# Optimization experiments

Hardware: AMD Instinct MI355X
Metric: run time of the kernel (lower is better)

Reference implementation:

```python
import jax, jax.numpy as jnp
import numpy as np

NUM_STEPS = 8  # fixed-step RK4 stand-in for adaptive DormandPrince(atol=1e-5)
B, D, C, H = 8192, 508, 1, 256
DIN = D + C + 1  # state + conditional + time


def _mlp(h, w0, b0, w1, b1, w2, b2):
    h = jnp.tanh(h @ w0 + b0)
    h = jnp.tanh(h @ w1 + b1)
    return h @ w2 + b2


def setup_inputs() -> dict:
    key = jax.random.key(0)
    ks = jax.random.split(key, 6)
    sc = lambda k, shape, fan: jax.random.normal(k, shape, jnp.float32) / np.sqrt(fan)
    return {
        "x": jax.random.normal(ks[0], (B, D), jnp.float32),
        "cond": jax.random.uniform(ks[1], (B, C), jnp.float32),
        "eps": jax.random.normal(ks[2], (B, D), jnp.float32),  # Hutchinson probe
        "w0": sc(ks[3], (DIN, H), DIN),
        "b0": jnp.zeros((H,), jnp.float32),
        "w1": sc(ks[4], (H, H), H),
        "b1": jnp.zeros((H,), jnp.float32),
        "w2": sc(ks[5], (H, D), H),
        "b2": jnp.zeros((D,), jnp.float32),
    }


def reference(x, cond, eps, w0, b0, w1, b1, w2, b2):
    """FFJORD bijector forward: integrate dx/dt = f(t, x, cond) from t=0 to 1
    with augmented Hutchinson trace estimate d(logdet)/dt = eps^T (df/dx) eps.
    Returns (y, log_det_jacobian_estimate)."""
    dt = jnp.float32(1.0 / NUM_STEPS)

    def dyn(t, y):
        def f(y_):
            tcol = jnp.full((y_.shape[0], 1), t, y_.dtype)
            return _mlp(jnp.concatenate([y_, cond, tcol], axis=-1),
                        w0, b0, w1, b1, w2, b2)
        fy, vjp_fn = jax.vjp(f, y)
        (etJ,) = vjp_fn(eps)           # eps^T J
        tr = jnp.sum(etJ * eps, -1)    # eps^T J eps  -> [B]
        return fy, tr

    def step(carry, i):
        y, ld = carry
        t = i * dt
        k1, l1 = dyn(t, y)
        k2, l2 = dyn(t + 0.5 * dt, y + 0.5 * dt * k1)
        k3, l3 = dyn(t + 0.5 * dt, y + 0.5 * dt * k2)
        k4, l4 = dyn(t + dt, y + dt * k3)
        y = y + (dt / 6.0) * (k1 + 2.0 * k2 + 2.0 * k3 + k4)
        ld = ld + (dt / 6.0) * (l1 + 2.0 * l2 + 2.0 * l3 + l4)
        return (y, ld), None

    init = (x, jnp.zeros((x.shape[0],), x.dtype))
    (y, ld), _ = jax.lax.scan(step, init, jnp.arange(NUM_STEPS, dtype=x.dtype))
    return y, ld
```

## Files before the change

### kernel.cpp

```cpp
#include <hip/hip_runtime.h>
#include <math.h>

namespace {

constexpr int Bn = 8192;
constexpr int Dn = 508;
constexpr int Hn = 256;
constexpr int NSTEPS = 8;
constexpr int Kp = 512;
constexpr float DT = 1.f / NSTEPS;
constexpr float DT6 = DT / 6.f;

typedef __attribute__((ext_vector_type(8))) short short8v;
typedef __attribute__((ext_vector_type(4))) float f32x4;

__device__ __forceinline__ short f2b(float f) {
  union { float f; unsigned u; } v; v.f = f;
  unsigned r = v.u + 0x7fffu + ((v.u >> 16) & 1u);
  return (short)(r >> 16);
}
__device__ __forceinline__ float b2f(short s) {
  union { unsigned u; float f; } v;
  v.u = ((unsigned)(unsigned short)s) << 16;
  return v.f;
}
__device__ __forceinline__ unsigned pk2(short lo, short hi) {
  return ((unsigned)(unsigned short)lo) | (((unsigned)(unsigned short)hi) << 16);
}
__device__ __forceinline__ float upk_lo(unsigned p) {
  union { unsigned u; float f; } v; v.u = p << 16; return v.f;
}
__device__ __forceinline__ float upk_hi(unsigned p) {
  union { unsigned u; float f; } v; v.u = p & 0xffff0000u; return v.f;
}
__device__ __forceinline__ float ftanh(float x) {
  x = fminf(fmaxf(x, -12.f), 12.f);
  const float e = __expf(2.f * x);
  return __fdividef(e - 1.f, e + 1.f);
}

template <int KT>
__device__ __forceinline__ void gemm_bb(const short* __restrict__ A, int lda,
                                        const short* __restrict__ Bt, int ldb,
                                        int row0, int col0, int lane,
                                        f32x4 acc[2][2]) {
  const int r = lane & 15, g = lane >> 4;
  const short* a0p = A + (size_t)(row0 + r) * lda + g * 8;
  const short* a1p = A + (size_t)(row0 + 16 + r) * lda + g * 8;
  const short* b0p = Bt + (size_t)(col0 + r) * ldb + g * 8;
  const short* b1p = Bt + (size_t)(col0 + 16 + r) * ldb + g * 8;
#pragma unroll
  for (int kt = 0; kt < KT; ++kt) {
    const short8v a0 = *(const short8v*)(a0p + kt * 32);
    const short8v a1 = *(const short8v*)(a1p + kt * 32);
    const short8v b0 = *(const short8v*)(b0p + kt * 32);
    const short8v b1 = *(const short8v*)(b1p + kt * 32);
    acc[0][0] = __builtin_amdgcn_mfma_f32_16x16x32_bf16(a0, b0, acc[0][0], 0, 0, 0);
    acc[0][1] = __builtin_amdgcn_mfma_f32_16x16x32_bf16(a0, b1, acc[0][1], 0, 0, 0);
    acc[1][0] = __builtin_amdgcn_mfma_f32_16x16x32_bf16(a1, b0, acc[1][0], 0, 0, 0);
    acc[1][1] = __builtin_amdgcn_mfma_f32_16x16x32_bf16(a1, b1, acc[1][1], 0, 0, 0);
  }
}

#define GEMM_PROLOGUE()                                     \
  const int tid = threadIdx.x, wid = tid >> 6, lane = tid & 63; \
  const int row0 = blockIdx.y * 64 + (wid >> 1) * 32;       \
  const int col0 = blockIdx.x * 64 + (wid & 1) * 32;        \
  const int rq = (lane >> 4) * 4, cc = lane & 15;           \
  const f32x4 z4 = {0.f, 0.f, 0.f, 0.f};                    \
  f32x4 acc[2][2] = {{z4, z4}, {z4, z4}};


__global__ __launch_bounds__(256) void k_cast_bf(const float* __restrict__ src, int R,
                                                 int C, short* __restrict__ dst, int ldd) {
  const int total = R * ldd;
  for (int idx = blockIdx.x * 256 + threadIdx.x; idx < total; idx += gridDim.x * 256) {
    const int r = idx / ldd, c = idx - r * ldd;
    dst[idx] = (c < C) ? f2b(src[(size_t)r * C + c]) : (short)0;
  }
}

__global__ __launch_bounds__(256) void k_transpose_bf(const float* __restrict__ src, int K,
                                                      int N, short* __restrict__ dst,
                                                      int Nd, int ldd) {
  const int total = Nd * ldd;
  for (int idx = blockIdx.x * 256 + threadIdx.x; idx < total; idx += gridDim.x * 256) {
    const int n = idx / ldd, k = idx - n * ldd;
    dst[idx] = (k < K && n < N) ? f2b(src[(size_t)k * N + n]) : (short)0;
  }
}

__global__ __launch_bounds__(256) void k_c0(const float* __restrict__ w0,
                                            const float* __restrict__ b2,
                                            float* __restrict__ c0) {
  const int n = threadIdx.x;
  float s = 0.f;
#pragma unroll 8
  for (int d = 0; d < Dn; ++d) s += b2[d] * w0[(size_t)d * Hn + n];
  c0[n] = s;
}

__global__ __launch_bounds__(256) void k_w20t(const short* __restrict__ w0T,
                                              const short* __restrict__ w2b,
                                              short* __restrict__ w20T) {
  GEMM_PROLOGUE();
  gemm_bb<16>(w0T, Kp, w2b, Kp, row0, col0, lane, acc);
#pragma unroll
  for (int i = 0; i < 2; ++i)
#pragma unroll
    for (int j = 0; j < 2; ++j)
#pragma unroll
      for (int q = 0; q < 4; ++q)
        w20T[(size_t)(row0 + i * 16 + rq + q) * Hn + col0 + j * 16 + cc] =
            f2b(acc[i][j][q]);
}

__global__ __launch_bounds__(256) void k_ginitx(const float* __restrict__ Af,
                                                const short* __restrict__ Bt,
                                                const float* __restrict__ cond,
                                                const float* __restrict__ w0c,
                                                float* __restrict__ zout) {
  GEMM_PROLOGUE();
  const int g = lane >> 4;
  const float* a0r = Af + (size_t)(row0 + cc) * Dn;
  const float* a1r = Af + (size_t)(row0 + 16 + cc) * Dn;
  const short* b0p = Bt + (size_t)(col0 + cc) * Kp + g * 8;
  const short* b1p = Bt + (size_t)(col0 + 16 + cc) * Kp + g * 8;
#pragma unroll
  for (int kt = 0; kt < 16; ++kt) {
    const int k = kt * 32 + g * 8;
    short8v a0v, a1v;
#pragma unroll
    for (int h = 0; h < 2; ++h) {
      const int k4 = k + h * 4;
      float4 fa = make_float4(0.f, 0.f, 0.f, 0.f);
      float4 fb = make_float4(0.f, 0.f, 0.f, 0.f);
      if (k4 < Dn) {
        fa = *(const float4*)(a0r + k4);
        fb = *(const float4*)(a1r + k4);
      }
      a0v[h * 4 + 0] = f2b(fa.x); a0v[h * 4 + 1] = f2b(fa.y);
      a0v[h * 4 + 2] = f2b(fa.z); a0v[h * 4 + 3] = f2b(fa.w);
      a1v[h * 4 + 0] = f2b(fb.x); a1v[h * 4 + 1] = f2b(fb.y);
      a1v[h * 4 + 2] = f2b(fb.z); a1v[h * 4 + 3] = f2b(fb.w);
    }
    const short8v b0v = *(const short8v*)(b0p + kt * 32);
    const short8v b1v = *(const short8v*)(b1p + kt * 32);
    acc[0][0] = __builtin_amdgcn_mfma_f32_16x16x32_bf16(a0v, b0v, acc[0][0], 0, 0, 0);
    acc[0][1] = __builtin_amdgcn_mfma_f32_16x16x32_bf16(a0v, b1v, acc[0][1], 0, 0, 0);
    acc[1][0] = __builtin_amdgcn_mfma_f32_16x16x32_bf16(a1v, b0v, acc[1][0], 0, 0, 0);
    acc[1][1] = __builtin_amdgcn_mfma_f32_16x16x32_bf16(a1v, b1v, acc[1][1], 0, 0, 0);
  }
#pragma unroll
  for (int i = 0; i < 2; ++i)
#pragma unroll
    for (int j = 0; j < 2; ++j)
#pragma unroll
      for (int q = 0; q < 4; ++q) {
        const int row = row0 + i * 16 + rq + q;
        const int col = col0 + j * 16 + cc;
        zout[(size_t)row * Hn + col] = acc[i][j][q] + cond[row] * w0c[col];
      }
}

__global__ __launch_bounds__(256) void k_giniteps(const float* __restrict__ Af,
                                                  const short* __restrict__ BtU,
                                                  const short* __restrict__ BtG,
                                                  short* __restrict__ uout,
                                                  short* __restrict__ gout) {
  GEMM_PROLOGUE();
  f32x4 acc2[2][2] = {{z4, z4}, {z4, z4}};
  const int g = lane >> 4;
  const float* a0r = Af + (size_t)(row0 + cc) * Dn;
  const float* a1r = Af + (size_t)(row0 + 16 + cc) * Dn;
  const short* u0p = BtU + (size_t)(col0 + cc) * Kp + g * 8;
  const short* u1p = BtU + (size_t)(col0 + 16 + cc) * Kp + g * 8;
  const short* g0p = BtG + (size_t)(col0 + cc) * Kp + g * 8;
  const short* g1p = BtG + (size_t)(col0 + 16 + cc) * Kp + g * 8;
#pragma unroll
  for (int kt = 0; kt < 16; ++kt) {
    const int k = kt * 32 + g * 8;
    short8v a0v, a1v;
#pragma unroll
    for (int h = 0; h < 2; ++h) {
      const int k4 = k + h * 4;
      float4 fa = make_float4(0.f, 0.f, 0.f, 0.f);
      float4 fb = make_float4(0.f, 0.f, 0.f, 0.f);
      if (k4 < Dn) {
        fa = *(const float4*)(a0r + k4);
        fb = *(const float4*)(a1r + k4);
      }
      a0v[h * 4 + 0] = f2b(fa.x); a0v[h * 4 + 1] = f2b(fa.y);
      a0v[h * 4 + 2] = f2b(fa.z); a0v[h * 4 + 3] = f2b(fa.w);
      a1v[h * 4 + 0] = f2b(fb.x); a1v[h * 4 + 1] = f2b(fb.y);
      a1v[h * 4 + 2] = f2b(fb.z); a1v[h * 4 + 3] = f2b(fb.w);
    }
    const short8v bu0 = *(const short8v*)(u0p + kt * 32);
    const short8v bu1 = *(const short8v*)(u1p + kt * 32);
    const short8v bg0 = *(const short8v*)(g0p + kt * 32);
    const short8v bg1 = *(const short8v*)(g1p + kt * 32);
    acc[0][0] = __builtin_amdgcn_mfma_f32_16x16x32_bf16(a0v, bu0, acc[0][0], 0, 0, 0);
    acc[0][1] = __builtin_amdgcn_mfma_f32_16x16x32_bf16(a0v, bu1, acc[0][1], 0, 0, 0);
    acc[1][0] = __builtin_amdgcn_mfma_f32_16x16x32_bf16(a1v, bu0, acc[1][0], 0, 0, 0);
    acc[1][1] = __builtin_amdgcn_mfma_f32_16x16x32_bf16(a1v, bu1, acc[1][1], 0, 0, 0);
    acc2[0][0] = __builtin_amdgcn_mfma_f32_16x16x32_bf16(a0v, bg0, acc2[0][0], 0, 0, 0);
    acc2[0][1] = __builtin_amdgcn_mfma_f32_16x16x32_bf16(a0v, bg1, acc2[0][1], 0, 0, 0);
    acc2[1][0] = __builtin_amdgcn_mfma_f32_16x16x32_bf16(a1v, bg0, acc2[1][0], 0, 0, 0);
    acc2[1][1] = __builtin_amdgcn_mfma_f32_16x16x32_bf16(a1v, bg1, acc2[1][1], 0, 0, 0);
  }
#pragma unroll
  for (int i = 0; i < 2; ++i)
#pragma unroll
    for (int j = 0; j < 2; ++j)
#pragma unroll
      for (int q = 0; q < 4; ++q) {
        const int row = row0 + i * 16 + rq + q;
        const int col = col0 + j * 16 + cc;
        uout[(size_t)row * Hn + col] = f2b(acc[i][j][q]);
        gout[(size_t)row * Hn + col] = f2b(acc2[i][j][q]);
      }
}

__global__ __launch_bounds__(256) void k_fragpack(const short* __restrict__ src,
                                                  short* __restrict__ dst, int total) {
  for (int idx = blockIdx.x * 256 + threadIdx.x; idx < total; idx += gridDim.x * 256) {
    const int j = idx & 7;
    const int l = (idx >> 3) & 63;
    const int ks = (idx >> 9) & 7;
    const int c16 = idx >> 12;
    dst[idx] = src[(size_t)(c16 * 16 + (l & 15)) * 256 + ks * 32 + (l >> 4) * 8 + j];
  }
}


__device__ __forceinline__ int swz(int row, int col) {
  return (row * 256 + col) ^ ((row & 7) << 3);
}

__global__ __launch_bounds__(512) void k_mega(
    const float* __restrict__ zg, const short* __restrict__ u_g,
    const short* __restrict__ g2_g, const short* __restrict__ w1P,
    const short* __restrict__ w20P, const short* __restrict__ w2P,
    const float* __restrict__ b0, const float* __restrict__ w0t,
    const float* __restrict__ b1, const float* __restrict__ c0,
    const float* __restrict__ b2, const float* __restrict__ x,
    float* __restrict__ yout, float* __restrict__ ldout) {
  __shared__ short As[32 * 256];
  __shared__ short h1s[16 * 256];
  __shared__ float red[16][8];

  const int tid = threadIdx.x;
  const int w = tid >> 6, lane = tid & 63;
  const int cc = lane & 15, g = lane >> 4, rq = g * 4;
  const int r0 = blockIdx.x * 16;
  const int cb = w * 32;

  float b0c[2], w0tc[2], b1c[2], c0c[2];
#pragma unroll
  for (int nt = 0; nt < 2; ++nt) {
    const int col = cb + nt * 16 + cc;
    b0c[nt] = b0[col];
    w0tc[nt] = w0t[col];
    b1c[nt] = b1[col];
    c0c[nt] = c0[col];
  }

  const short* w1base = w1P + (size_t)(2 * w) * 4096 + lane * 8;
  const short* w20base = w20P + (size_t)(2 * w) * 4096 + lane * 8;

  const size_t gbase = (size_t)(r0 + rq) * Hn + cb + cc;

  float z_[2][4], kzp[2][4], kza[2][4], hs[2][4], tr_[4];
  unsigned u_pk[2][2], g2_pk[2][2];
#pragma unroll
  for (int nt = 0; nt < 2; ++nt) {
    const size_t i0 = gbase + nt * 16;
#pragma unroll
    for (int q = 0; q < 4; ++q) {
      z_[nt][q] = zg[i0 + (size_t)q * Hn];
      kzp[nt][q] = 0.f;
      hs[nt][q] = 0.f;
    }
    u_pk[nt][0] = pk2(u_g[i0], u_g[i0 + Hn]);
    u_pk[nt][1] = pk2(u_g[i0 + 2 * Hn], u_g[i0 + 3 * Hn]);
    g2_pk[nt][0] = pk2(g2_g[i0], g2_g[i0 + Hn]);
    g2_pk[nt][1] = pk2(g2_g[i0 + 2 * Hn], g2_g[i0 + 3 * Hn]);
  }
#pragma unroll
  for (int q = 0; q < 4; ++q) tr_[q] = 0.f;

  const f32x4 zero4 = {0.f, 0.f, 0.f, 0.f};

#pragma unroll 1
  for (int e = 0; e < 4 * NSTEPS; ++e) {
    const int j = e & 3, s = e >> 2;
    const float oj = (j == 0) ? 0.f : ((j == 3) ? 1.f : 0.5f);
    const float aj = (j == 0) ? 0.f : ((j == 3) ? DT : 0.5f * DT);
    const float mj = (j == 1 || j == 2) ? 2.f : 1.f;
    const float tval = ((float)s + oj) * DT;

#pragma unroll
    for (int nt = 0; nt < 2; ++nt)
#pragma unroll
      for (int q = 0; q < 4; ++q) {
        const int row = rq + q;
        const int colh = cb + nt * 16 + cc;
        const float pre = z_[nt][q] + aj * kzp[nt][q] + b0c[nt] + tval * w0tc[nt];
        const float h = ftanh(pre);
        const float uq = (q & 1) ? upk_hi(u_pk[nt][q >> 1]) : upk_lo(u_pk[nt][q >> 1]);
        As[swz(row, colh)] = f2b(h);
        As[swz(16 + row, colh)] = f2b((1.f - h * h) * uq);
      }
    __syncthreads();

    {
      f32x4 acc[2][2] = {{zero4, zero4}, {zero4, zero4}};
#pragma unroll
      for (int ks = 0; ks < 8; ++ks) {
        const short8v b0v = *(const short8v*)(w1base + ks * 512);
        const short8v b1v = *(const short8v*)(w1base + 4096 + ks * 512);
        const short8v a0 = *(const short8v*)(As + swz(cc, g * 8 + ks * 32));
        const short8v a1 = *(const short8v*)(As + swz(16 + cc, g * 8 + ks * 32));
        acc[0][0] = __builtin_amdgcn_mfma_f32_16x16x32_bf16(a0, b0v, acc[0][0], 0, 0, 0);
        acc[0][1] = __builtin_amdgcn_mfma_f32_16x16x32_bf16(a0, b1v, acc[0][1], 0, 0, 0);
        acc[1][0] = __builtin_amdgcn_mfma_f32_16x16x32_bf16(a1, b0v, acc[1][0], 0, 0, 0);
        acc[1][1] = __builtin_amdgcn_mfma_f32_16x16x32_bf16(a1, b1v, acc[1][1], 0, 0, 0);
      }
#pragma unroll
      for (int nt = 0; nt < 2; ++nt)
#pragma unroll
        for (int q = 0; q < 4; ++q) {
          const float v = ftanh(acc[0][nt][q] + b1c[nt]);
          const float g2q =
              (q & 1) ? upk_hi(g2_pk[nt][q >> 1]) : upk_lo(g2_pk[nt][q >> 1]);
          tr_[q] += (DT6 * mj) * g2q * (1.f - v * v) * acc[1][nt][q];
          h1s[swz(rq + q, cb + nt * 16 + cc)] = f2b(v);
          hs[nt][q] += mj * v;
        }
    }
    __syncthreads();

    {
      f32x4 acc2[2] = {zero4, zero4};
#pragma unroll
      for (int ks = 0; ks < 8; ++ks) {
        const short8v b0v = *(const short8v*)(w20base + ks * 512);
        const short8v b1v = *(const short8v*)(w20base + 4096 + ks * 512);
        const short8v a = *(const short8v*)(h1s + swz(cc, g * 8 + ks * 32));
        acc2[0] = __builtin_amdgcn_mfma_f32_16x16x32_bf16(a, b0v, acc2[0], 0, 0, 0);
        acc2[1] = __builtin_amdgcn_mfma_f32_16x16x32_bf16(a, b1v, acc2[1], 0, 0, 0);
      }
#pragma unroll
      for (int nt = 0; nt < 2; ++nt)
#pragma unroll
        for (int q = 0; q < 4; ++q) {
          const float kzv = acc2[nt][q] + c0c[nt];
          if (j == 0) {
            kza[nt][q] = kzv;
            kzp[nt][q] = kzv;
          } else if (j < 3) {
            kza[nt][q] += mj * kzv;
            kzp[nt][q] = kzv;
          } else {
            z_[nt][q] += DT6 * (kza[nt][q] + kzv);
          }
        }
    }
  }

#pragma unroll
  for (int nt = 0; nt < 2; ++nt)
#pragma unroll
    for (int q = 0; q < 4; ++q)
      As[swz(rq + q, cb + nt * 16 + cc)] = f2b(hs[nt][q]);
  __syncthreads();
  {
    const short* w2base = w2P + (size_t)(4 * w) * 4096 + lane * 8;
    f32x4 facc[4] = {zero4, zero4, zero4, zero4};
#pragma unroll
    for (int ks = 0; ks < 8; ++ks) {
      const short8v a = *(const short8v*)(As + swz(cc, g * 8 + ks * 32));
#pragma unroll
      for (int nt = 0; nt < 4; ++nt) {
        const short8v bv = *(const short8v*)(w2base + nt * 4096 + ks * 512);
        facc[nt] = __builtin_amdgcn_mfma_f32_16x16x32_bf16(a, bv, facc[nt], 0, 0, 0);
      }
    }
#pragma unroll
    for (int nt = 0; nt < 4; ++nt) {
      const int colo = w * 64 + nt * 16 + cc;
      if (colo < Dn) {
        const float b2c = b2[colo];
#pragma unroll
        for (int q = 0; q < 4; ++q) {
          const size_t ix = (size_t)(r0 + rq + q) * Dn + colo;
          yout[ix] = x[ix] + DT6 * facc[nt][q] + b2c;
        }
      }
    }
  }

#pragma unroll
  for (int q = 0; q < 4; ++q) {
    float v = tr_[q];
    v += __shfl_xor(v, 1);
    v += __shfl_xor(v, 2);
    v += __shfl_xor(v, 4);
    v += __shfl_xor(v, 8);
    if (cc == 0) red[rq + q][w] = v;
  }
  __syncthreads();
  if (tid < 16) {
    float t = 0.f;
#pragma unroll
    for (int ww = 0; ww < 8; ++ww) t += red[tid][ww];
    ldout[r0 + tid] = t;
  }
}

}

extern "C" void kernel_launch(void* const* d_in, const int* in_sizes, int n_in,
                              void* d_out, int out_size, void* d_ws, size_t ws_size,
                              hipStream_t stream) {
  const float* x = (const float*)d_in[0];
  const float* cond = (const float*)d_in[1];
  const float* eps = (const float*)d_in[2];
  const float* w0 = (const float*)d_in[3];
  const float* b0 = (const float*)d_in[4];
  const float* w1 = (const float*)d_in[5];
  const float* b1 = (const float*)d_in[6];
  const float* w2 = (const float*)d_in[7];
  const float* b2 = (const float*)d_in[8];
  const float* w0c = w0 + (size_t)508 * Hn;
  const float* w0t = w0 + (size_t)509 * Hn;

  const size_t BD = (size_t)Bn * Dn, BH = (size_t)Bn * Hn;
  char* p = (char*)d_ws;
  auto alloc_f = [&](size_t n) { float* r = (float*)p; p += n * 4; return r; };
  auto alloc_s = [&](size_t n) { short* r = (short*)p; p += ((n * 2 + 15) & ~15ull); return r; };

  float* zg = alloc_f(BH);
  float* c0 = alloc_f(256);
  short* u_g = alloc_s(BH);
  short* g2_g = alloc_s(BH);
  short* w0T = alloc_s(256 * 512);
  short* w1T = alloc_s(256 * 256);
  short* w2b = alloc_s(256 * 512);
  short* w2T = alloc_s(512 * 256);
  short* w20T = alloc_s(256 * 256);
  short* w1P = alloc_s(256 * 256);
  short* w20P = alloc_s(256 * 256);
  short* w2P = alloc_s(512 * 256);

  float* yout = (float*)d_out;
  float* ldout = (float*)d_out + BD;

  const dim3 blk(256);
  const dim3 gH(Hn / 64, Bn / 64);
  const dim3 gW(4, 4);

  k_cast_bf<<<512, blk, 0, stream>>>(w2, Hn, Dn, w2b, Kp);
  k_transpose_bf<<<256, blk, 0, stream>>>(w1, Hn, Hn, w1T, Hn, Hn);
  k_transpose_bf<<<512, blk, 0, stream>>>(w0, Dn, Hn, w0T, Hn, Kp);
  k_transpose_bf<<<512, blk, 0, stream>>>(w2, Hn, Dn, w2T, Kp, Hn);
  k_c0<<<1, blk, 0, stream>>>(w0, b2, c0);
  k_w20t<<<gW, blk, 0, stream>>>(w0T, w2b, w20T);
  k_ginitx<<<gH, blk, 0, stream>>>(x, w0T, cond, w0c, zg);
  k_giniteps<<<gH, blk, 0, stream>>>(eps, w0T, w2b, u_g, g2_g);
  k_fragpack<<<256, blk, 0, stream>>>(w1T, w1P, 256 * 256);
  k_fragpack<<<256, blk, 0, stream>>>(w20T, w20P, 256 * 256);
  k_fragpack<<<512, blk, 0, stream>>>(w2T, w2P, 512 * 256);

  k_mega<<<dim3(Bn / 16), dim3(512), 0, stream>>>(zg, u_g, g2_g, w1P, w20P,
                                                  w2P, b0, w0t, b1, c0, b2, x,
                                                  yout, ldout);
}
```

Measured before the change: 306.5 us.

## Process 32 rows per block to reuse weight fragments across two row tiles

Each block of the fused ODE kernel now handles 32 batch rows instead of 16, so every weight fragment loaded from global memory for the W1 and W20 MFMAs serves two row tiles. The running hidden-state sum moves from registers into a padded shared-memory array to hold down register pressure from the doubled per-thread state. The grid halves to 256 blocks, which may leave some compute units idle or lower occupancy, and the larger LDS footprint (about 33KB for hsum alone) limits how many blocks fit per CU.

```diff
diff --git a/kernel.cpp b/kernel.cpp
--- a/kernel.cpp
+++ b/kernel.cpp
@@ -237,6 +237,8 @@
   return (row * 256 + col) ^ ((row & 7) << 3);
 }
 
+constexpr int HP = 258;
+
 __global__ __launch_bounds__(512) void k_mega(
     const float* __restrict__ zg, const short* __restrict__ u_g,
     const short* __restrict__ g2_g, const short* __restrict__ w1P,
@@ -245,14 +247,15 @@
     const float* __restrict__ b1, const float* __restrict__ c0,
     const float* __restrict__ b2, const float* __restrict__ x,
     float* __restrict__ yout, float* __restrict__ ldout) {
-  __shared__ short As[32 * 256];
-  __shared__ short h1s[16 * 256];
-  __shared__ float red[16][8];
+  __shared__ short As[64 * 256];
+  __shared__ short h1s[32 * 256];
+  __shared__ float hsum[32 * HP];
+  __shared__ float red[32][8];
 
   const int tid = threadIdx.x;
   const int w = tid >> 6, lane = tid & 63;
   const int cc = lane & 15, g = lane >> 4, rq = g * 4;
-  const int r0 = blockIdx.x * 16;
+  const int r0 = blockIdx.x * 32;
   const int cb = w * 32;
 
   float b0c[2], w0tc[2], b1c[2], c0c[2];
@@ -270,24 +273,29 @@
 
   const size_t gbase = (size_t)(r0 + rq) * Hn + cb + cc;
 
-  float z_[2][4], kzp[2][4], kza[2][4], hs[2][4], tr_[4];
-  unsigned u_pk[2][2], g2_pk[2][2];
-#pragma unroll
-  for (int nt = 0; nt < 2; ++nt) {
-    const size_t i0 = gbase + nt * 16;
-#pragma unroll
-    for (int q = 0; q < 4; ++q) {
-      z_[nt][q] = zg[i0 + (size_t)q * Hn];
-      kzp[nt][q] = 0.f;
-      hs[nt][q] = 0.f;
-    }
-    u_pk[nt][0] = pk2(u_g[i0], u_g[i0 + Hn]);
-    u_pk[nt][1] = pk2(u_g[i0 + 2 * Hn], u_g[i0 + 3 * Hn]);
-    g2_pk[nt][0] = pk2(g2_g[i0], g2_g[i0 + Hn]);
-    g2_pk[nt][1] = pk2(g2_g[i0 + 2 * Hn], g2_g[i0 + 3 * Hn]);
-  }
-#pragma unroll
-  for (int q = 0; q < 4; ++q) tr_[q] = 0.f;
+  float z_[2][2][4], kzp[2][2][4], kza[2][2][4], tr_[2][4];
+  unsigned u_pk[2][2][2], g2_pk[2][2][2];
+#pragma unroll
+  for (int rb = 0; rb < 2; ++rb)
+#pragma unroll
+    for (int nt = 0; nt < 2; ++nt) {
+      const size_t i0 = gbase + (size_t)(rb * 16) * Hn + nt * 16;
+#pragma unroll
+      for (int q = 0; q < 4; ++q) {
+        z_[rb][nt][q] = zg[i0 + (size_t)q * Hn];
+        kzp[rb][nt][q] = 0.f;
+      }
+      u_pk[rb][nt][0] = pk2(u_g[i0], u_g[i0 + Hn]);
+      u_pk[rb][nt][1] = pk2(u_g[i0 + 2 * Hn], u_g[i0 + 3 * Hn]);
+      g2_pk[rb][nt][0] = pk2(g2_g[i0], g2_g[i0 + Hn]);
+      g2_pk[rb][nt][1] = pk2(g2_g[i0 + 2 * Hn], g2_g[i0 + 3 * Hn]);
+    }
+#pragma unroll
+  for (int rb = 0; rb < 2; ++rb)
+#pragma unroll
+    for (int q = 0; q < 4; ++q) tr_[rb][q] = 0.f;
+
+  for (int i = tid; i < 32 * HP; i += 512) hsum[i] = 0.f;
 
   const f32x4 zero4 = {0.f, 0.f, 0.f, 0.f};
 
@@ -300,27 +308,33 @@
     const float tval = ((float)s + oj) * DT;
 
 #pragma unroll
-    for (int nt = 0; nt < 2; ++nt)
-#pragma unroll
-      for (int q = 0; q < 4; ++q) {
-        const int row = rq + q;
-        const int colh = cb + nt * 16 + cc;
-        const float pre = z_[nt][q] + aj * kzp[nt][q] + b0c[nt] + tval * w0tc[nt];
-        const float h = ftanh(pre);
-        const float uq = (q & 1) ? upk_hi(u_pk[nt][q >> 1]) : upk_lo(u_pk[nt][q >> 1]);
-        As[swz(row, colh)] = f2b(h);
-        As[swz(16 + row, colh)] = f2b((1.f - h * h) * uq);
-      }
+    for (int rb = 0; rb < 2; ++rb)
+#pragma unroll
+      for (int nt = 0; nt < 2; ++nt)
+#pragma unroll
+        for (int q = 0; q < 4; ++q) {
+          const int row = rb * 16 + rq + q;
+          const int colh = cb + nt * 16 + cc;
+          const float pre =
+              z_[rb][nt][q] + aj * kzp[rb][nt][q] + b0c[nt] + tval * w0tc[nt];
+          const float h = ftanh(pre);
+          const float uq = (q & 1) ? upk_hi(u_pk[rb][nt][q >> 1])
+                                   : upk_lo(u_pk[rb][nt][q >> 1]);
+          As[swz(row, colh)] = f2b(h);
+          As[swz(32 + row, colh)] = f2b((1.f - h * h) * uq);
+        }
     __syncthreads();
 
-    {
+#pragma unroll
+    for (int rb = 0; rb < 2; ++rb) {
       f32x4 acc[2][2] = {{zero4, zero4}, {zero4, zero4}};
 #pragma unroll
       for (int ks = 0; ks < 8; ++ks) {
         const short8v b0v = *(const short8v*)(w1base + ks * 512);
         const short8v b1v = *(const short8v*)(w1base + 4096 + ks * 512);
-        const short8v a0 = *(const short8v*)(As + swz(cc, g * 8 + ks * 32));
-        const short8v a1 = *(const short8v*)(As + swz(16 + cc, g * 8 + ks * 32));
+        const short8v a0 = *(const short8v*)(As + swz(rb * 16 + cc, g * 8 + ks * 32));
+        const short8v a1 =
+            *(const short8v*)(As + swz(32 + rb * 16 + cc, g * 8 + ks * 32));
         acc[0][0] = __builtin_amdgcn_mfma_f32_16x16x32_bf16(a0, b0v, acc[0][0], 0, 0, 0);
         acc[0][1] = __builtin_amdgcn_mfma_f32_16x16x32_bf16(a0, b1v, acc[0][1], 0, 0, 0);
         acc[1][0] = __builtin_amdgcn_mfma_f32_16x16x32_bf16(a1, b0v, acc[1][0], 0, 0, 0);
@@ -331,55 +345,68 @@
 #pragma unroll
         for (int q = 0; q < 4; ++q) {
           const float v = ftanh(acc[0][nt][q] + b1c[nt]);
-          const float g2q =
-              (q & 1) ? upk_hi(g2_pk[nt][q >> 1]) : upk_lo(g2_pk[nt][q >> 1]);
-          tr_[q] += (DT6 * mj) * g2q * (1.f - v * v) * acc[1][nt][q];
-          h1s[swz(rq + q, cb + nt * 16 + cc)] = f2b(v);
-          hs[nt][q] += mj * v;
+          const float g2q = (q & 1) ? upk_hi(g2_pk[rb][nt][q >> 1])
+                                    : upk_lo(g2_pk[rb][nt][q >> 1]);
+          tr_[rb][q] += (DT6 * mj) * g2q * (1.f - v * v) * acc[1][nt][q];
+          const int row = rb * 16 + rq + q;
+          const int colh = cb + nt * 16 + cc;
+          h1s[swz(row, colh)] = f2b(v);
+          hsum[row * HP + colh] += mj * v;
         }
     }
     __syncthreads();
 
     {
-      f32x4 acc2[2] = {zero4, zero4};
+      f32x4 acc2[2][2] = {{zero4, zero4}, {zero4, zero4}};
 #pragma unroll
       for (int ks = 0; ks < 8; ++ks) {
         const short8v b0v = *(const short8v*)(w20base + ks * 512);
         const short8v b1v = *(const short8v*)(w20base + 4096 + ks * 512);
-        const short8v a = *(const short8v*)(h1s + swz(cc, g * 8 + ks * 32));
-        acc2[0] = __builtin_amdgcn_mfma_f32_16x16x32_bf16(a, b0v, acc2[0], 0, 0, 0);
-        acc2[1] = __builtin_amdgcn_mfma_f32_16x16x32_bf16(a, b1v, acc2[1], 0, 0, 0);
-      }
-#pragma unroll
-      for (int nt = 0; nt < 2; ++nt)
-#pragma unroll
-        for (int q = 0; q < 4; ++q) {
-          const float kzv = acc2[nt][q] + c0c[nt];
-          if (j == 0) {
-            kza[nt][q] = kzv;
-            kzp[nt][q] = kzv;
-          } else if (j < 3) {
-            kza[nt][q] += mj * kzv;
-            kzp[nt][q] = kzv;
-          } else {
-            z_[nt][q] += DT6 * (kza[nt][q] + kzv);
+        const short8v a0 = *(const short8v*)(h1s + swz(cc, g * 8 + ks * 32));
+        const short8v a1 = *(const short8v*)(h1s + swz(16 + cc, g * 8 + ks * 32));
+        acc2[0][0] = __builtin_amdgcn_mfma_f32_16x16x32_bf16(a0, b0v, acc2[0][0], 0, 0, 0);
+        acc2[0][1] = __builtin_amdgcn_mfma_f32_16x16x32_bf16(a0, b1v, acc2[0][1], 0, 0, 0);
+        acc2[1][0] = __builtin_amdgcn_mfma_f32_16x16x32_bf16(a1, b0v, acc2[1][0], 0, 0, 0);
+        acc2[1][1] = __builtin_amdgcn_mfma_f32_16x16x32_bf16(a1, b1v, acc2[1][1], 0, 0, 0);
+      }
+#pragma unroll
+      for (int rb = 0; rb < 2; ++rb)
+#pragma unroll
+        for (int nt = 0; nt < 2; ++nt)
+#pragma unroll
+          for (int q = 0; q < 4; ++q) {
+            const float kzv = acc2[rb][nt][q] + c0c[nt];
+            if (j == 0) {
+              kza[rb][nt][q] = kzv;
+              kzp[rb][nt][q] = kzv;
+            } else if (j < 3) {
+              kza[rb][nt][q] += mj * kzv;
+              kzp[rb][nt][q] = kzv;
+            } else {
+              z_[rb][nt][q] += DT6 * (kza[rb][nt][q] + kzv);
+            }
           }
-        }
-    }
-  }
-
-#pragma unroll
-  for (int nt = 0; nt < 2; ++nt)
-#pragma unroll
-    for (int q = 0; q < 4; ++q)
-      As[swz(rq + q, cb + nt * 16 + cc)] = f2b(hs[nt][q]);
+    }
+  }
+
+#pragma unroll
+  for (int rb = 0; rb < 2; ++rb)
+#pragma unroll
+    for (int nt = 0; nt < 2; ++nt)
+#pragma unroll
+      for (int q = 0; q < 4; ++q) {
+        const int row = rb * 16 + rq + q;
+        const int colh = cb + nt * 16 + cc;
+        As[swz(row, colh)] = f2b(hsum[row * HP + colh]);
+      }
   __syncthreads();
-  {
+#pragma unroll 1
+  for (int rb = 0; rb < 2; ++rb) {
     const short* w2base = w2P + (size_t)(4 * w) * 4096 + lane * 8;
     f32x4 facc[4] = {zero4, zero4, zero4, zero4};
 #pragma unroll
     for (int ks = 0; ks < 8; ++ks) {
-      const short8v a = *(const short8v*)(As + swz(cc, g * 8 + ks * 32));
+      const short8v a = *(const short8v*)(As + swz(rb * 16 + cc, g * 8 + ks * 32));
 #pragma unroll
       for (int nt = 0; nt < 4; ++nt) {
         const short8v bv = *(const short8v*)(w2base + nt * 4096 + ks * 512);
@@ -393,7 +420,7 @@
         const float b2c = b2[colo];
 #pragma unroll
         for (int q = 0; q < 4; ++q) {
-          const size_t ix = (size_t)(r0 + rq + q) * Dn + colo;
+          const size_t ix = (size_t)(r0 + rb * 16 + rq + q) * Dn + colo;
           yout[ix] = x[ix] + DT6 * facc[nt][q] + b2c;
         }
       }
@@ -401,16 +428,18 @@
   }
 
 #pragma unroll
-  for (int q = 0; q < 4; ++q) {
-    float v = tr_[q];
-    v += __shfl_xor(v, 1);
-    v += __shfl_xor(v, 2);
-    v += __shfl_xor(v, 4);
-    v += __shfl_xor(v, 8);
-    if (cc == 0) red[rq + q][w] = v;
-  }
+  for (int rb = 0; rb < 2; ++rb)
+#pragma unroll
+    for (int q = 0; q < 4; ++q) {
+      float v = tr_[rb][q];
+      v += __shfl_xor(v, 1);
+      v += __shfl_xor(v, 2);
+      v += __shfl_xor(v, 4);
+      v += __shfl_xor(v, 8);
+      if (cc == 0) red[rb * 16 + rq + q][w] = v;
+    }
   __syncthreads();
-  if (tid < 16) {
+  if (tid < 32) {
     float t = 0.f;
 #pragma unroll
     for (int ww = 0; ww < 8; ++ww) t += red[tid][ww];
@@ -472,7 +501,7 @@
   k_fragpack<<<256, blk, 0, stream>>>(w20T, w20P, 256 * 256);
   k_fragpack<<<512, blk, 0, stream>>>(w2T, w2P, 512 * 256);
 
-  k_mega<<<dim3(Bn / 16), dim3(512), 0, stream>>>(zg, u_g, g2_g, w1P, w20P,
+  k_mega<<<dim3(Bn / 32), dim3(512), 0, stream>>>(zg, u_g, g2_g, w1P, w20P,
                                                   w2P, b0, w0t, b1, c0, b2, x,
                                                   yout, ldout);
 }
```

New measurement: 1.198 ms. 291% more time.
